# Performance work log

Hardware: AMD Instinct MI355X
Metric: run time of the kernel (lower is better)

Reference implementation:

```python
import jax, jax.numpy as jnp
from jax import lax
import numpy as np

GROUPS = 4


def _grid_sample_border(img, gx, gy):
    # img: [Bg, Cg, H, W]; gx, gy: [Bg, H, W] normalized grid in [-1, 1]
    # Replicates F.grid_sample(mode='bilinear', align_corners=False, padding_mode='border')
    Bg, Cg, H, W = img.shape
    ix = jnp.clip(((gx + 1.0) * W - 1.0) * 0.5, 0.0, W - 1.0)
    iy = jnp.clip(((gy + 1.0) * H - 1.0) * 0.5, 0.0, H - 1.0)
    x0 = jnp.floor(ix)
    y0 = jnp.floor(iy)
    wx = ix - x0
    wy = iy - y0
    x0i = x0.astype(jnp.int32)
    y0i = y0.astype(jnp.int32)
    x1i = jnp.minimum(x0i + 1, W - 1)
    y1i = jnp.minimum(y0i + 1, H - 1)

    def one(im, x0i, x1i, y0i, y1i, wx, wy):
        v00 = im[:, y0i, x0i]
        v01 = im[:, y0i, x1i]
        v10 = im[:, y1i, x0i]
        v11 = im[:, y1i, x1i]
        return (v00 * (1 - wx) * (1 - wy) + v01 * wx * (1 - wy)
                + v10 * (1 - wx) * wy + v11 * wx * wy)

    return jax.vmap(one)(img, x0i, x1i, y0i, y1i, wx, wy)


def setup_inputs() -> dict:
    key = jax.random.key(0)
    ks = jax.random.split(key, 8)
    B, N, C = 8, 4096, 768
    x = jax.random.normal(ks[0], (B, N, C), dtype=jnp.float32)
    dw_w = jax.random.normal(ks[1], (C, 1, 3, 3), dtype=jnp.float32) * 0.1  # depthwise kernel
    dw_b = jax.random.normal(ks[2], (C,), dtype=jnp.float32) * 0.1
    off_w = jax.random.normal(ks[3], (2 * GROUPS, C), dtype=jnp.float32) * 0.001  # std=0.001 init
    off_b = jnp.zeros((2 * GROUPS,), dtype=jnp.float32)
    wt_w = jax.random.normal(ks[4], (2 * GROUPS, C), dtype=jnp.float32) * 0.02
    wt_b = jnp.zeros((2 * GROUPS,), dtype=jnp.float32)
    offset_list = jnp.zeros((1,), dtype=jnp.int32)
    return {"x": x, "dw_w": dw_w, "dw_b": dw_b, "off_w": off_w, "off_b": off_b,
            "wt_w": wt_w, "wt_b": wt_b, "offset_list": offset_list,
            "patch_h": 64, "patch_w": 64}


def reference(x, dw_w, dw_b, off_w, off_b, wt_w, wt_b, offset_list, patch_h, patch_w):
    B, N, C = x.shape
    H, W = int(patch_h), int(patch_w)
    xi = jnp.transpose(x, (0, 2, 1)).reshape(B, C, H, W)

    # offset head: depthwise 3x3 conv -> GELU -> 1x1 conv to 2*groups channels
    dw = lax.conv_general_dilated(xi, dw_w, (1, 1), ((1, 1), (1, 1)),
                                  dimension_numbers=("NCHW", "OIHW", "NCHW"),
                                  feature_group_count=C)
    dw = jax.nn.gelu(dw + dw_b[None, :, None, None], approximate=False)
    off = jnp.einsum("bchw,oc->bohw", dw, off_w) + off_b[None, :, None, None]

    # weight head: 1x1 conv -> sigmoid
    wt = jax.nn.sigmoid(jnp.einsum("bchw,oc->bohw", xi, wt_w) + wt_b[None, :, None, None])

    off = (off * wt).reshape(B, 2, GROUPS, H, W)
    # fixed cross-shaped shifts: x-comp [0,0,-1,+1], y-comp [-1,+1,0,0]
    shifts = jnp.array([[0.0, 0.0, -1.0, 1.0], [-1.0, 1.0, 0.0, 0.0]],
                       dtype=x.dtype).reshape(1, 2, GROUPS, 1, 1)
    off = off + shifts

    cx = (jnp.arange(W, dtype=x.dtype) + 0.5)[None, None, None, :]  # pixel-center x coords
    cy = (jnp.arange(H, dtype=x.dtype) + 0.5)[None, None, :, None]  # pixel-center y coords
    gx = 2.0 * (cx + off[:, 0]) / W - 1.0  # [B, GROUPS, H, W]
    gy = 2.0 * (cy + off[:, 1]) / H - 1.0

    img = xi.reshape(B * GROUPS, C // GROUPS, H, W)
    samp = _grid_sample_border(img, gx.reshape(B * GROUPS, H, W),
                               gy.reshape(B * GROUPS, H, W))
    out = samp.reshape(B, C, N)
    return jnp.transpose(out, (0, 2, 1))  # [B, N, C]
```

## Files before the change

kernel.cpp:

```cpp
#include <hip/hip_runtime.h>
#include <math.h>

#define BB 8
#define CC 768
#define HH 64
#define WW 64
#define NN 4096
#define GG 4
#define NCHUNK 6
#define CHUNK 128

typedef __attribute__((ext_vector_type(8))) _Float16 half8;
typedef __attribute__((ext_vector_type(4))) float f32x4;

__device__ __forceinline__ float gelu_fast(float v) {
    const float z = 1.5957691216f * v * fmaf(0.044715f, v * v, 1.0f);
    return __fdividef(v, 1.0f + __expf(-z));
}

__global__ __launch_bounds__(128, 4) void dq_conv_mfma(
    const float* __restrict__ x,
    const float* __restrict__ dw_w,
    const float* __restrict__ dw_b,
    const float* __restrict__ off_w,
    const float* __restrict__ wt_w,
    float* __restrict__ offpart)
{
    __shared__ __attribute__((aligned(16))) _Float16 gl[2][16][144];
    const int t = threadIdx.x;
    const int lane = t & 63, wv = t >> 6;
    const int xcd = blockIdx.x & 7;
    const int local = blockIdx.x >> 3;
    const int chunk = local % NCHUNK;
    const int r = xcd * (BB * HH / 8) + local / NCHUNK;
    const int h = r & (HH - 1);
    const int b = r >> 6;
    const int c = chunk * CHUNK + t;

    const int n = lane & 15, kg = lane >> 4;
    const float* wsrc = (wv == 0) ? off_w : wt_w;
    half8 bfrag[4];
#pragma unroll
    for (int kt = 0; kt < 4; ++kt) {
        const bool valid = (n < 8);
        const float* src = wsrc + (valid ? n : 0) * CC + chunk * CHUNK + kt * 32 + kg * 8;
        half8 bf;
#pragma unroll
        for (int j = 0; j < 8; ++j) {
            const float v = valid ? src[j] : 0.f;
            bf[j] = (_Float16)v;
        }
        bfrag[kt] = bf;
    }

    float w9[9];
#pragma unroll
    for (int j = 0; j < 9; ++j) w9[j] = dw_w[c * 9 + j];
    const float bias = dw_b[c];
    const bool tv = (h > 0), bv = (h < HH - 1);
    const float wt0 = tv ? w9[0] : 0.f, wt1 = tv ? w9[1] : 0.f, wt2 = tv ? w9[2] : 0.f;
    const float wb0 = bv ? w9[6] : 0.f, wb1 = bv ? w9[7] : 0.f, wb2 = bv ? w9[8] : 0.f;

    const float* base = x + (size_t)b * NN * CC + c;
    const float* rT = base + (size_t)((tv ? h - 1 : 0) * WW) * CC;
    const float* rM = base + (size_t)(h * WW) * CC;
    const float* rB = base + (size_t)((bv ? h + 1 : h) * WW) * CC;

    const float* xq1 = x + ((size_t)(b * NN + h * WW + n)) * CC + chunk * CHUNK + kg * 8;

    float cT[8], cM[8], cB[8], nT[8], nM[8], nB[8];
    float pT = 0.f, pM = 0.f, pB = 0.f;

#pragma unroll
    for (int j = 0; j < 8; ++j) {
        const size_t o = (size_t)j * CC;
        cT[j] = rT[o]; cM[j] = rM[o]; cB[j] = rB[o];
    }

#pragma unroll
    for (int q = 0; q < 4; ++q) {
        const int qb = q & 1;
#pragma unroll
        for (int hb = 0; hb < 2; ++hb) {
            const int wb = q * 2 + hb;
            if (wb < 7) {
#pragma unroll
                for (int j = 0; j < 8; ++j) {
                    const size_t o = (size_t)(wb * 8 + 8 + j) * CC;
                    nT[j] = rT[o]; nM[j] = rM[o]; nB[j] = rB[o];
                }
            } else {
#pragma unroll
                for (int j = 0; j < 8; ++j) { nT[j] = 0.f; nM[j] = 0.f; nB[j] = 0.f; }
            }
#pragma unroll
            for (int j = 0; j < 8; ++j) {
                const float lT = j ? cT[j - 1] : pT;
                const float lM = j ? cM[j - 1] : pM;
                const float lB = j ? cB[j - 1] : pB;
                const float rTv = (j == 7) ? nT[0] : cT[j + 1];
                const float rMv = (j == 7) ? nM[0] : cM[j + 1];
                const float rBv = (j == 7) ? nB[0] : cB[j + 1];
                const float conv = lT * wt0 + cT[j] * wt1 + rTv * wt2
                                 + lM * w9[3] + cM[j] * w9[4] + rMv * w9[5]
                                 + lB * wb0 + cB[j] * wb1 + rBv * wb2;
                gl[qb][hb * 8 + j][t] = (_Float16)gelu_fast(conv + bias);
            }
            pT = cT[7]; pM = cM[7]; pB = cB[7];
#pragma unroll
            for (int j = 0; j < 8; ++j) { cT[j] = nT[j]; cM[j] = nM[j]; cB[j] = nB[j]; }
        }

        __syncthreads();
        f32x4 acc = {0.f, 0.f, 0.f, 0.f};
        if (wv == 0) {
#pragma unroll
            for (int kt = 0; kt < 4; ++kt) {
                const half8 a = *(const half8*)&gl[qb][n][kt * 32 + kg * 8];
                acc = __builtin_amdgcn_mfma_f32_16x16x32_f16(a, bfrag[kt], acc, 0, 0, 0);
            }
        } else {
            const float* xp = xq1 + (size_t)(q * 16) * CC;
#pragma unroll
            for (int kt = 0; kt < 4; ++kt) {
                const float4 va = *(const float4*)(xp + kt * 32);
                const float4 vb = *(const float4*)(xp + kt * 32 + 4);
                half8 a;
                a[0] = (_Float16)va.x; a[1] = (_Float16)va.y;
                a[2] = (_Float16)va.z; a[3] = (_Float16)va.w;
                a[4] = (_Float16)vb.x; a[5] = (_Float16)vb.y;
                a[6] = (_Float16)vb.z; a[7] = (_Float16)vb.w;
                acc = __builtin_amdgcn_mfma_f32_16x16x32_f16(a, bfrag[kt], acc, 0, 0, 0);
            }
        }
        if (n < 8) {
            const int plane = chunk * 16 + (wv ? 8 + n : n);
            const size_t gpos = (size_t)(b * NN) + h * WW + q * 16 + kg * 4;
            float4 st; st.x = acc[0]; st.y = acc[1]; st.z = acc[2]; st.w = acc[3];
            *(float4*)&offpart[(size_t)plane * (BB * NN) + gpos] = st;
        }
    }
}

__global__ __launch_bounds__(256) void dq_combine(
    const float* __restrict__ offpart,
    const float* __restrict__ off_b,
    const float* __restrict__ wt_b,
    float* __restrict__ ixiy)
{
    const int t = threadIdx.x;
    const int o = t >> 5;
    const int gpos = blockIdx.x * 32 + (t & 31);
    const int b = gpos >> 12;
    const int hw = gpos & 4095;
    const int h = hw >> 6, w = hw & 63;

    float so = 0.f, sw = 0.f;
#pragma unroll
    for (int ch = 0; ch < NCHUNK; ++ch) {
        so += offpart[((size_t)(ch * 16 + o)) * (BB * NN) + gpos];
        sw += offpart[((size_t)(ch * 16 + 8 + o)) * (BB * NN) + gpos];
    }
    const float sig = 1.f / (1.f + __expf(-(sw + wt_b[o])));
    const float val = (so + off_b[o]) * sig;

    if (o < 4) {
        const float shx = (o == 2) ? -1.f : ((o == 3) ? 1.f : 0.f);
        const float ix = fminf(fmaxf((float)w + val + shx, 0.f), (float)(WW - 1));
        ixiy[(b * GG + o) * NN + hw] = ix;
    } else {
        const int g = o - 4;
        const float shy = (g == 0) ? -1.f : ((g == 1) ? 1.f : 0.f);
        const float iy = fminf(fmaxf((float)h + val + shy, 0.f), (float)(HH - 1));
        ixiy[BB * GG * NN + (b * GG + g) * NN + hw] = iy;
    }
}

__global__ __launch_bounds__(192) void dq_sample_vec(
    const float* __restrict__ x,
    const float* __restrict__ ixiy,
    float* __restrict__ out)
{
    __shared__ float ixy[8];
    const int t = threadIdx.x;
    const int p = (blockIdx.x & 7) * (BB * NN / 8) + (blockIdx.x >> 3);
    const int b = p >> 12;
    const int hw = p & 4095;

    if (t < 8) {
        const int g = t & 3;
        const int plane = (t >> 2) * (BB * GG * NN);
        ixy[t] = ixiy[plane + (b * GG + g) * NN + hw];
    }
    __syncthreads();

    const int g = t / 48;
    const float ix = ixy[g], iy = ixy[4 + g];
    const float x0f = floorf(ix), y0f = floorf(iy);
    const float wx = ix - x0f, wy = iy - y0f;
    const int x0 = (int)x0f, y0 = (int)y0f;
    const int x1 = min(x0 + 1, WW - 1), y1 = min(y0 + 1, HH - 1);
    const int c4 = t * 4;
    const float* xb = x + (size_t)b * NN * CC;
    const float4 v00 = *(const float4*)(xb + (size_t)(y0 * WW + x0) * CC + c4);
    const float4 v01 = *(const float4*)(xb + (size_t)(y0 * WW + x1) * CC + c4);
    const float4 v10 = *(const float4*)(xb + (size_t)(y1 * WW + x0) * CC + c4);
    const float4 v11 = *(const float4*)(xb + (size_t)(y1 * WW + x1) * CC + c4);
    const float w00 = (1.f - wx) * (1.f - wy), w01 = wx * (1.f - wy);
    const float w10 = (1.f - wx) * wy,         w11 = wx * wy;
    float4 r;
    r.x = v00.x * w00 + v01.x * w01 + v10.x * w10 + v11.x * w11;
    r.y = v00.y * w00 + v01.y * w01 + v10.y * w10 + v11.y * w11;
    r.z = v00.z * w00 + v01.z * w01 + v10.z * w10 + v11.z * w11;
    r.w = v00.w * w00 + v01.w * w01 + v10.w * w10 + v11.w * w11;
    *(float4*)(out + (size_t)p * CC + c4) = r;
}

__global__ __launch_bounds__(256) void dqshift_offsets_kernel(
    const float* __restrict__ x, const float* __restrict__ dw_w,
    const float* __restrict__ dw_b, const float* __restrict__ off_w,
    const float* __restrict__ off_b, const float* __restrict__ wt_w,
    const float* __restrict__ wt_b, float* __restrict__ ixiy)
{
    const int wave = threadIdx.x >> 6;
    const int lane = threadIdx.x & 63;
    const int p = blockIdx.x * 4 + wave;
    const int b = p >> 12;
    const int hw = p & 4095;
    const int h = hw >> 6;
    const int w = hw & 63;
    const float* xb = x + (size_t)b * NN * CC;
    float accO[8], accW[8];
#pragma unroll
    for (int o = 0; o < 8; ++o) { accO[o] = 0.f; accW[o] = 0.f; }
    for (int k = 0; k < CC / 64; ++k) {
        const int c = lane + (k << 6);
        float conv = 0.f, xc = 0.f;
#pragma unroll
        for (int dy = -1; dy <= 1; ++dy) {
            const int hh = h + dy;
            const bool vy = (hh >= 0) && (hh < HH);
#pragma unroll
            for (int dx = -1; dx <= 1; ++dx) {
                const int ww = w + dx;
                const bool vv = vy && (ww >= 0) && (ww < WW);
                const float tt = vv ? xb[(size_t)(hh * WW + ww) * CC + c] : 0.f;
                if (dy == 0 && dx == 0) xc = tt;
                conv = fmaf(tt, dw_w[c * 9 + (dy + 1) * 3 + (dx + 1)], conv);
            }
        }
        const float gv = conv + dw_b[c];
        const float gle = 0.5f * gv * (1.0f + erff(gv * 0.70710678118654752f));
#pragma unroll
        for (int o = 0; o < 8; ++o) {
            accO[o] = fmaf(gle, off_w[o * CC + c], accO[o]);
            accW[o] = fmaf(xc, wt_w[o * CC + c], accW[o]);
        }
    }
#pragma unroll
    for (int o = 0; o < 8; ++o) {
#pragma unroll
        for (int s = 32; s > 0; s >>= 1) {
            accO[o] += __shfl_xor(accO[o], s, 64);
            accW[o] += __shfl_xor(accW[o], s, 64);
        }
    }
    if (lane == 0) {
        const float shx[4] = {0.f, 0.f, -1.f, 1.f};
        const float shy[4] = {-1.f, 1.f, 0.f, 0.f};
#pragma unroll
        for (int g = 0; g < 4; ++g) {
            const float sx = 1.f / (1.f + expf(-(accW[g] + wt_b[g])));
            const float sy = 1.f / (1.f + expf(-(accW[4 + g] + wt_b[4 + g])));
            const float ox = (accO[g] + off_b[g]) * sx + shx[g];
            const float oy = (accO[4 + g] + off_b[4 + g]) * sy + shy[g];
            const float ix = fminf(fmaxf((float)w + ox, 0.f), (float)(WW - 1));
            const float iy = fminf(fmaxf((float)h + oy, 0.f), (float)(HH - 1));
            const int idx = (b * GG + g) * NN + hw;
            ixiy[idx] = ix;
            ixiy[BB * GG * NN + idx] = iy;
        }
    }
}

__global__ __launch_bounds__(256) void dqshift_sample_kernel(
    const float* __restrict__ x,
    const float* __restrict__ ixiy,
    float* __restrict__ out)
{
    const int p = blockIdx.x;
    const int b = p >> 12;
    const int hw = p & 4095;
    const float* xb = x + (size_t)b * NN * CC;
    float* ob = out + (size_t)p * CC;

#pragma unroll
    for (int k = 0; k < 3; ++k) {
        const int c = threadIdx.x + (k << 8);
        const int g = c / (CC / GG);
        const int idx = (b * GG + g) * NN + hw;
        const float ix = ixiy[idx];
        const float iy = ixiy[BB * GG * NN + idx];
        const float x0f = floorf(ix);
        const float y0f = floorf(iy);
        const float wx = ix - x0f;
        const float wy = iy - y0f;
        const int x0 = (int)x0f;
        const int y0 = (int)y0f;
        const int x1 = min(x0 + 1, WW - 1);
        const int y1 = min(y0 + 1, HH - 1);
        const float* r0 = xb + (size_t)(y0 * WW) * CC + c;
        const float* r1 = xb + (size_t)(y1 * WW) * CC + c;
        const float v00 = r0[(size_t)x0 * CC];
        const float v01 = r0[(size_t)x1 * CC];
        const float v10 = r1[(size_t)x0 * CC];
        const float v11 = r1[(size_t)x1 * CC];
        ob[c] = v00 * (1.f - wx) * (1.f - wy) + v01 * wx * (1.f - wy)
              + v10 * (1.f - wx) * wy + v11 * wx * wy;
    }
}

extern "C" void kernel_launch(void* const* d_in, const int* in_sizes, int n_in,
                              void* d_out, int out_size, void* d_ws, size_t ws_size,
                              hipStream_t stream) {
    const float* x     = (const float*)d_in[0];
    const float* dw_w  = (const float*)d_in[1];
    const float* dw_b  = (const float*)d_in[2];
    const float* off_w = (const float*)d_in[3];
    const float* off_b = (const float*)d_in[4];
    const float* wt_w  = (const float*)d_in[5];
    const float* wt_b  = (const float*)d_in[6];

    float* ixiy = (float*)d_ws;
    float* offpart = (float*)d_ws + 2 * BB * GG * NN;
    const size_t need = (size_t)(2 * BB * GG * NN + NCHUNK * 16 * BB * NN) * 4;

    if (ws_size >= need) {
        dq_conv_mfma<<<BB * HH * NCHUNK, 128, 0, stream>>>(
            x, dw_w, dw_b, off_w, wt_w, offpart);
        dq_combine<<<BB * NN / 32, 256, 0, stream>>>(
            offpart, off_b, wt_b, ixiy);
        dq_sample_vec<<<BB * NN, 192, 0, stream>>>(
            x, ixiy, (float*)d_out);
    } else {
        dqshift_offsets_kernel<<<BB * NN / 4, 256, 0, stream>>>(
            x, dw_w, dw_b, off_w, off_b, wt_w, wt_b, ixiy);
        dqshift_sample_kernel<<<BB * NN, 256, 0, stream>>>(x, ixiy, (float*)d_out);
    }
}
```

Baseline: 82.52 us.

## Use single-wave conv blocks that reuse loaded center row for weight-head MFMA

The conv kernel now runs one 64-thread wave per block over 64-channel chunks, doubling the chunk count. The same wave computes both the offset-head and weight-head MFMAs. The weight head's input comes from the center-row values already held in registers, staged as fp16 in shared memory, so x is no longer reloaded from global memory. This drops the __syncthreads and the double-buffered LDS. In exchange it doubles the partial planes that dq_combine must read, and each block does a serial LDS write then read without an explicit barrier.

```diff
diff --git a/kernel.cpp b/kernel.cpp
--- a/kernel.cpp
+++ b/kernel.cpp
@@ -7,8 +7,8 @@
 #define WW 64
 #define NN 4096
 #define GG 4
-#define NCHUNK 6
-#define CHUNK 128
+#define NCHUNK 12
+#define CHUNK 64
 
 typedef __attribute__((ext_vector_type(8))) _Float16 half8;
 typedef __attribute__((ext_vector_type(4))) float f32x4;
@@ -18,7 +18,7 @@
     return __fdividef(v, 1.0f + __expf(-z));
 }
 
-__global__ __launch_bounds__(128, 4) void dq_conv_mfma(
+__global__ __launch_bounds__(64, 8) void dq_conv_mfma(
     const float* __restrict__ x,
     const float* __restrict__ dw_w,
     const float* __restrict__ dw_b,
@@ -26,9 +26,9 @@
     const float* __restrict__ wt_w,
     float* __restrict__ offpart)
 {
-    __shared__ __attribute__((aligned(16))) _Float16 gl[2][16][144];
+    __shared__ __attribute__((aligned(16))) _Float16 gl[16][72];
+    __shared__ __attribute__((aligned(16))) _Float16 xh[16][72];
     const int t = threadIdx.x;
-    const int lane = t & 63, wv = t >> 6;
     const int xcd = blockIdx.x & 7;
     const int local = blockIdx.x >> 3;
     const int chunk = local % NCHUNK;
@@ -37,20 +37,21 @@
     const int b = r >> 6;
     const int c = chunk * CHUNK + t;
 
-    const int n = lane & 15, kg = lane >> 4;
-    const float* wsrc = (wv == 0) ? off_w : wt_w;
-    half8 bfrag[4];
-#pragma unroll
-    for (int kt = 0; kt < 4; ++kt) {
+    const int n = t & 15, kg = t >> 4;
+    half8 bfo[2], bfw[2];
+#pragma unroll
+    for (int kt = 0; kt < 2; ++kt) {
         const bool valid = (n < 8);
-        const float* src = wsrc + (valid ? n : 0) * CC + chunk * CHUNK + kt * 32 + kg * 8;
-        half8 bf;
+        const int co = chunk * CHUNK + kt * 32 + kg * 8;
+        const float* so = off_w + (valid ? n : 0) * CC + co;
+        const float* sw = wt_w + (valid ? n : 0) * CC + co;
+        half8 fo, fw;
 #pragma unroll
         for (int j = 0; j < 8; ++j) {
-            const float v = valid ? src[j] : 0.f;
-            bf[j] = (_Float16)v;
-        }
-        bfrag[kt] = bf;
+            fo[j] = (_Float16)(valid ? so[j] : 0.f);
+            fw[j] = (_Float16)(valid ? sw[j] : 0.f);
+        }
+        bfo[kt] = fo; bfw[kt] = fw;
     }
 
     float w9[9];
@@ -66,8 +67,6 @@
     const float* rM = base + (size_t)(h * WW) * CC;
     const float* rB = base + (size_t)((bv ? h + 1 : h) * WW) * CC;
 
-    const float* xq1 = x + ((size_t)(b * NN + h * WW + n)) * CC + chunk * CHUNK + kg * 8;
-
     float cT[8], cM[8], cB[8], nT[8], nM[8], nB[8];
     float pT = 0.f, pM = 0.f, pB = 0.f;
 
@@ -79,7 +78,6 @@
 
 #pragma unroll
     for (int q = 0; q < 4; ++q) {
-        const int qb = q & 1;
 #pragma unroll
         for (int hb = 0; hb < 2; ++hb) {
             const int wb = q * 2 + hb;
@@ -104,40 +102,30 @@
                 const float conv = lT * wt0 + cT[j] * wt1 + rTv * wt2
                                  + lM * w9[3] + cM[j] * w9[4] + rMv * w9[5]
                                  + lB * wb0 + cB[j] * wb1 + rBv * wb2;
-                gl[qb][hb * 8 + j][t] = (_Float16)gelu_fast(conv + bias);
+                const int colq = hb * 8 + j;
+                gl[colq][t] = (_Float16)gelu_fast(conv + bias);
+                xh[colq][t] = (_Float16)cM[j];
             }
             pT = cT[7]; pM = cM[7]; pB = cB[7];
 #pragma unroll
             for (int j = 0; j < 8; ++j) { cT[j] = nT[j]; cM[j] = nM[j]; cB[j] = nB[j]; }
         }
 
-        __syncthreads();
-        f32x4 acc = {0.f, 0.f, 0.f, 0.f};
-        if (wv == 0) {
-#pragma unroll
-            for (int kt = 0; kt < 4; ++kt) {
-                const half8 a = *(const half8*)&gl[qb][n][kt * 32 + kg * 8];
-                acc = __builtin_amdgcn_mfma_f32_16x16x32_f16(a, bfrag[kt], acc, 0, 0, 0);
-            }
-        } else {
-            const float* xp = xq1 + (size_t)(q * 16) * CC;
-#pragma unroll
-            for (int kt = 0; kt < 4; ++kt) {
-                const float4 va = *(const float4*)(xp + kt * 32);
-                const float4 vb = *(const float4*)(xp + kt * 32 + 4);
-                half8 a;
-                a[0] = (_Float16)va.x; a[1] = (_Float16)va.y;
-                a[2] = (_Float16)va.z; a[3] = (_Float16)va.w;
-                a[4] = (_Float16)vb.x; a[5] = (_Float16)vb.y;
-                a[6] = (_Float16)vb.z; a[7] = (_Float16)vb.w;
-                acc = __builtin_amdgcn_mfma_f32_16x16x32_f16(a, bfrag[kt], acc, 0, 0, 0);
-            }
+        f32x4 accO = {0.f, 0.f, 0.f, 0.f};
+        f32x4 accW = {0.f, 0.f, 0.f, 0.f};
+#pragma unroll
+        for (int kt = 0; kt < 2; ++kt) {
+            const half8 ag = *(const half8*)&gl[n][kt * 32 + kg * 8];
+            accO = __builtin_amdgcn_mfma_f32_16x16x32_f16(ag, bfo[kt], accO, 0, 0, 0);
+            const half8 ax = *(const half8*)&xh[n][kt * 32 + kg * 8];
+            accW = __builtin_amdgcn_mfma_f32_16x16x32_f16(ax, bfw[kt], accW, 0, 0, 0);
         }
         if (n < 8) {
-            const int plane = chunk * 16 + (wv ? 8 + n : n);
             const size_t gpos = (size_t)(b * NN) + h * WW + q * 16 + kg * 4;
-            float4 st; st.x = acc[0]; st.y = acc[1]; st.z = acc[2]; st.w = acc[3];
-            *(float4*)&offpart[(size_t)plane * (BB * NN) + gpos] = st;
+            float4 so; so.x = accO[0]; so.y = accO[1]; so.z = accO[2]; so.w = accO[3];
+            float4 sw; sw.x = accW[0]; sw.y = accW[1]; sw.z = accW[2]; sw.w = accW[3];
+            *(float4*)&offpart[(size_t)(chunk * 16 + n) * (BB * NN) + gpos] = so;
+            *(float4*)&offpart[(size_t)(chunk * 16 + 8 + n) * (BB * NN) + gpos] = sw;
         }
     }
 }
@@ -336,7 +324,7 @@
     const size_t need = (size_t)(2 * BB * GG * NN + NCHUNK * 16 * BB * NN) * 4;
 
     if (ws_size >= need) {
-        dq_conv_mfma<<<BB * HH * NCHUNK, 128, 0, stream>>>(
+        dq_conv_mfma<<<BB * HH * NCHUNK, CHUNK, 0, stream>>>(
             x, dw_w, dw_b, off_w, wt_w, offpart);
         dq_combine<<<BB * NN / 32, 256, 0, stream>>>(
             offpart, off_b, wt_b, ixiy);
```

Result: slower. 142.2 us (+72.3%).
